# Kernel optimization log

Hardware: AMD Instinct MI355X
Metric: run time of the kernel (lower is better)

Reference implementation:

```python
import jax, jax.numpy as jnp
import numpy as np

NEG = -1e30  # log-zero surrogate (avoid -inf for stable grads)


def ctc_neg_log_like(log_probs, targets, input_lengths, target_lengths):
    """Standard CTC (blank=0) negative log-likelihood, mean over batch.
    Math-equivalent to k2 topo-compile + intersect_dense + log-semiring tot_scores.
    log_probs: [B,T,C] logits or log-probs (re-normalized, as GradExpNormalize does).
    """
    lp = jax.nn.log_softmax(log_probs, axis=-1)
    B, T, C = lp.shape
    S = targets.shape[1]
    L = 2 * S + 1  # blank-interleaved extended label sequence length
    ext = jnp.zeros((B, L), jnp.int32).at[:, 1::2].set(targets.astype(jnp.int32))
    prev2 = jnp.pad(ext[:, :-2], ((0, 0), (2, 0)), constant_values=-1)
    can_skip = (ext != prev2) & (ext != 0)  # skip transition allowed

    lp_tb = jnp.moveaxis(lp, 1, 0)  # [T,B,C] for scan over time
    start = jnp.full((B, L), NEG, lp.dtype).at[:, 0].set(0.0).at[:, 1].set(0.0)
    alpha0 = start + jnp.take_along_axis(lp_tb[0], ext, axis=1)  # [B,L]

    def step(alpha, xs):
        lp_t, t = xs
        emit_t = jnp.take_along_axis(lp_t, ext, axis=1)  # [B,L]
        s1 = jnp.pad(alpha[:, :-1], ((0, 0), (1, 0)), constant_values=NEG)
        s2 = jnp.where(can_skip,
                       jnp.pad(alpha[:, :-2], ((0, 0), (2, 0)), constant_values=NEG),
                       NEG)
        new = jnp.logaddexp(jnp.logaddexp(alpha, s1), s2) + emit_t
        # freeze alpha once past this utterance's length
        new = jnp.where((t < input_lengths)[:, None], new, alpha)
        return new, None

    ts = jnp.arange(1, T, dtype=jnp.int32)
    alpha, _ = jax.lax.scan(step, alpha0, (lp_tb[1:], ts))

    idx1 = (2 * target_lengths).astype(jnp.int32)
    idx2 = jnp.maximum(2 * target_lengths - 1, 0).astype(jnp.int32)
    a1 = jnp.take_along_axis(alpha, idx1[:, None], axis=1)[:, 0]
    a2 = jnp.take_along_axis(alpha, idx2[:, None], axis=1)[:, 0]
    a2 = jnp.where(target_lengths > 0, a2, NEG)
    tot_scores = jnp.logaddexp(a1, a2)  # per-utterance log-likelihood
    return -jnp.mean(tot_scores)  # reduction='mean'


def setup_inputs() -> dict:
    key = jax.random.key(0)
    k1, k2, k3, k4 = jax.random.split(key, 4)
    B, T, C, S = 64, 2048, 1024, 256
    log_probs = jax.random.normal(k1, (B, T, C), dtype=jnp.float32)
    targets = 1 + jax.random.randint(k2, (B, S), 0, C - 1, dtype=jnp.int32)  # labels in [1, C)
    input_lengths = jax.random.randint(k3, (B,), T // 2, T + 1, dtype=jnp.int32)
    target_lengths = jax.random.randint(k4, (B,), S // 2, S + 1, dtype=jnp.int32)
    return {"log_probs": log_probs, "targets": targets,
            "input_lengths": input_lengths, "target_lengths": target_lengths}


def reference(log_probs, targets, input_lengths, target_lengths):
    return ctc_neg_log_like(log_probs, targets, input_lengths, target_lengths)
```

## Files before the change

kernel.cpp:

```cpp
#include <hip/hip_runtime.h>
#include <math.h>

typedef __attribute__((ext_vector_type(4))) float f32x4;

#define SB() __builtin_amdgcn_sched_barrier(0)
#define WAITV(n)                                              \
  do {                                                        \
    asm volatile("s_waitcnt vmcnt(" #n ")" ::: "memory");     \
    SB();                                                     \
  } while (0)
#define LD4(dst, ptr, OFF)                                           \
  asm volatile("global_load_dwordx4 %0, %1, off offset:" OFF         \
               : "=v"(dst) : "v"(ptr) : "memory")
#define LD1(dst, ptr, OFF)                                           \
  asm volatile("global_load_dword %0, %1, off offset:" OFF           \
               : "=v"(dst) : "v"(ptr) : "memory")

__device__ inline float wave_max64(float v) {
#pragma unroll
  for (int off = 32; off > 0; off >>= 1) v = fmaxf(v, __shfl_xor(v, off, 64));
  return v;
}
__device__ inline float wave_sum64(float v) {
#pragma unroll
  for (int off = 32; off > 0; off >>= 1) v += __shfl_xor(v, off, 64);
  return v;
}
__device__ inline float wave_max_dpp(float x) {
  int xi = __float_as_int(x);
  x = fmaxf(x, __int_as_float(__builtin_amdgcn_update_dpp(xi, xi, 0x111, 0xf, 0xf, false)));
  xi = __float_as_int(x);
  x = fmaxf(x, __int_as_float(__builtin_amdgcn_update_dpp(xi, xi, 0x112, 0xf, 0xf, false)));
  xi = __float_as_int(x);
  x = fmaxf(x, __int_as_float(__builtin_amdgcn_update_dpp(xi, xi, 0x114, 0xf, 0xf, false)));
  xi = __float_as_int(x);
  x = fmaxf(x, __int_as_float(__builtin_amdgcn_update_dpp(xi, xi, 0x118, 0xf, 0xf, false)));
  xi = __float_as_int(x);
  x = fmaxf(x, __int_as_float(__builtin_amdgcn_update_dpp(xi, xi, 0x142, 0xa, 0xf, false)));
  xi = __float_as_int(x);
  x = fmaxf(x, __int_as_float(__builtin_amdgcn_update_dpp(xi, xi, 0x143, 0xc, 0xf, false)));
  return __int_as_float(__builtin_amdgcn_readlane(__float_as_int(x), 63));
}
__device__ inline float lane_shr1(float x) {
  return __int_as_float(__builtin_amdgcn_update_dpp(
      0, __float_as_int(x), 0x138, 0xf, 0xf, true));
}

__device__ __forceinline__ void k1_body(
    const float* __restrict__ lp, const int* __restrict__ targets,
    float* __restrict__ gw, int t0, int T, int Tc, int CB, int S,
    int b, int tq, float* rowbuf) {
  const int lane = threadIdx.x & 63;
  const int w = threadIdx.x >> 6;
  const int tloc = tq * 4 + w;
  const int t = t0 + tloc;
  if (t >= T) return;
  const int4 tg4 = *(const int4*)(targets + (size_t)b * S + 4 * lane);

  const float* row = lp + ((size_t)b * T + t) * 1024;
  const float4 v0 = *(const float4*)(row + 4 * lane);
  const float4 v1 = *(const float4*)(row + 256 + 4 * lane);
  const float4 v2 = *(const float4*)(row + 512 + 4 * lane);
  const float4 v3 = *(const float4*)(row + 768 + 4 * lane);
  float mx = fmaxf(fmaxf(fmaxf(v0.x, v0.y), fmaxf(v0.z, v0.w)),
                   fmaxf(fmaxf(v1.x, v1.y), fmaxf(v1.z, v1.w)));
  mx = fmaxf(mx, fmaxf(fmaxf(fmaxf(v2.x, v2.y), fmaxf(v2.z, v2.w)),
                       fmaxf(fmaxf(v3.x, v3.y), fmaxf(v3.z, v3.w))));
  mx = wave_max64(mx);
  float sm = __expf(v0.x - mx) + __expf(v0.y - mx) + __expf(v0.z - mx) +
             __expf(v0.w - mx) + __expf(v1.x - mx) + __expf(v1.y - mx) +
             __expf(v1.z - mx) + __expf(v1.w - mx) + __expf(v2.x - mx) +
             __expf(v2.y - mx) + __expf(v2.z - mx) + __expf(v2.w - mx) +
             __expf(v3.x - mx) + __expf(v3.y - mx) + __expf(v3.z - mx) +
             __expf(v3.w - mx);
  sm = wave_sum64(sm);
  const float lse = mx + __logf(sm);
  *(float4*)(rowbuf + 4 * lane) = v0;
  *(float4*)(rowbuf + 256 + 4 * lane) = v1;
  *(float4*)(rowbuf + 512 + 4 * lane) = v2;
  *(float4*)(rowbuf + 768 + 4 * lane) = v3;
  const float e0 = __expf(rowbuf[tg4.x] - lse);
  const float e1 = __expf(rowbuf[tg4.y] - lse);
  const float e2 = __expf(rowbuf[tg4.z] - lse);
  const float e3 = __expf(rowbuf[tg4.w] - lse);
  float* gr = gw + ((size_t)b * CB + tloc) * 272;
  *(float4*)(gr + 4 * lane) = make_float4(e0, e1, e2, e3);
  if (lane == 0) gr[256] = __expf(rowbuf[0] - lse);
}

__global__ __launch_bounds__(256) void k1_std(
    const float* __restrict__ lp, const int* __restrict__ targets,
    float* __restrict__ gw, int t0, int T, int Tc, int CB, int S) {
  __shared__ __align__(16) float rowbuf4[4][1024];
  k1_body(lp, targets, gw, t0, T, Tc, CB, S, blockIdx.y, blockIdx.x,
          rowbuf4[threadIdx.x >> 6]);
}

#define DECL8(P)                                                     \
  f32x4 P##v0, P##v1, P##v2, P##v3, P##v4, P##v5, P##v6, P##v7;      \
  float P##q0, P##q1, P##q2, P##q3, P##q4, P##q5, P##q6, P##q7;

#define ISS8(P)                                                      \
  do {                                                               \
    LD4(P##v0, gpA_, "0");    LD1(P##q0, gqA_, "0");                 \
    LD4(P##v1, gpA_, "1088"); LD1(P##q1, gqA_, "1088");              \
    LD4(P##v2, gpA_, "2176"); LD1(P##q2, gqA_, "2176");              \
    LD4(P##v3, gpA_, "3264"); LD1(P##q3, gqA_, "3264");              \
    LD4(P##v4, gpB_, "0");    LD1(P##q4, gqB_, "0");                 \
    LD4(P##v5, gpB_, "1088"); LD1(P##q5, gqB_, "1088");              \
    LD4(P##v6, gpB_, "2176"); LD1(P##q6, gqB_, "2176");              \
    LD4(P##v7, gpB_, "3264"); LD1(P##q7, gqB_, "3264");              \
    gpA_ += 2176; gqA_ += 2176; gpB_ += 2176; gqB_ += 2176;          \
  } while (0)

#define KSR(pv, qv)                                              \
  {                                                              \
    const float hm1 = lane_shr1(a7);                             \
    const float n0 = (a0 + hm1) * (qv);                          \
    const float n1 = __fmaf_rn(sk1, hm1, a1 + a0) * (pv).x;      \
    const float n2 = (a2 + a1) * (qv);                           \
    const float n3 = __fmaf_rn(sk3, a1, a3 + a2) * (pv).y;       \
    const float n4 = (a4 + a3) * (qv);                           \
    const float n5 = __fmaf_rn(sk5, a3, a5 + a4) * (pv).z;       \
    const float n6 = (a6 + a5) * (qv);                           \
    const float n7 = __fmaf_rn(sk7, a5, a7 + a6) * (pv).w;       \
    const float n8 = (a8 + a7) * (qv);                           \
    a0 = n0; a1 = n1; a2 = n2; a3 = n3; a4 = n4;                 \
    a5 = n5; a6 = n6; a7 = n7; a8 = n8;                          \
  }

#define RESC()                                                            \
  {                                                                       \
    float m_ = fmaxf(fmaxf(fmaxf(fmaxf(a0, a1), fmaxf(a2, a3)),           \
                           fmaxf(fmaxf(a4, a5), fmaxf(a6, a7))), a8);     \
    m_ = wave_max_dpp(m_);                                                \
    const int e_ =                                                        \
        (m_ > 0.f) ? (int)((__float_as_uint(m_) >> 23) & 255u) - 127 : 0; \
    a0 = ldexpf(a0, -e_); a1 = ldexpf(a1, -e_); a2 = ldexpf(a2, -e_);     \
    a3 = ldexpf(a3, -e_); a4 = ldexpf(a4, -e_); a5 = ldexpf(a5, -e_);     \
    a6 = ldexpf(a6, -e_); a7 = ldexpf(a7, -e_); a8 = ldexpf(a8, -e_);     \
    E += e_;                                                              \
  }

#define COMP8(P, rem)                                            \
  do {                                                           \
    if ((rem) >= 8) {                                            \
      KSR(P##v0, P##q0) KSR(P##v1, P##q1) KSR(P##v2, P##q2)      \
      KSR(P##v3, P##q3) KSR(P##v4, P##q4) KSR(P##v5, P##q5)      \
      KSR(P##v6, P##q6) KSR(P##v7, P##q7) RESC()                 \
    } else {                                                     \
      KSR(P##v0, P##q0)                                          \
      if ((rem) > 1) KSR(P##v1, P##q1)                           \
      if ((rem) > 2) KSR(P##v2, P##q2)                           \
      if ((rem) > 3) KSR(P##v3, P##q3)                           \
      if ((rem) > 4) KSR(P##v4, P##q4)                           \
      if ((rem) > 5) KSR(P##v5, P##q5)                           \
      if ((rem) > 6) KSR(P##v6, P##q6)                           \
      RESC()                                                     \
    }                                                            \
  } while (0)

template <int R0, int LAST>
__device__ __forceinline__ void k2_body(
    const float* __restrict__ gb, const int* __restrict__ targets,
    const int* __restrict__ in_len, const int* __restrict__ tgt_len,
    float* __restrict__ alpha_g, int* __restrict__ exp_g,
    float* __restrict__ tot, int b, int t0, int Tc, int S) {
  const int lane = threadIdx.x & 63;
  const int len = in_len[b];
  const int tl = tgt_len[b];
  const int* tg = targets + (size_t)b * S;
  const int4 mytg = *(const int4*)(tg + 4 * lane);
  const int tgm1 = (lane > 0) ? tg[4 * lane - 1] : -1;
  const float sk1 = (lane > 0 && mytg.x != tgm1) ? 1.f : 0.f;
  const float sk3 = (mytg.y != mytg.x) ? 1.f : 0.f;
  const float sk5 = (mytg.z != mytg.y) ? 1.f : 0.f;
  const float sk7 = (mytg.w != mytg.z) ? 1.f : 0.f;

  float a0 = 0.f, a1 = 0.f, a2 = 0.f, a3 = 0.f, a4 = 0.f, a5 = 0.f, a6 = 0.f,
        a7 = 0.f, a8 = 0.f;
  int E = 0;
  if (R0) {
    if (lane == 0) { a0 = gb[256]; a1 = gb[0]; }
  } else {
    const float* ap = alpha_g + (size_t)b * 520 + 8 * lane;
    a0 = ap[0]; a1 = ap[1]; a2 = ap[2]; a3 = ap[3];
    a4 = ap[4]; a5 = ap[5]; a6 = ap[6]; a7 = ap[7];
    a8 = (lane == 63) ? alpha_g[(size_t)b * 520 + 512] : 0.f;
    E = exp_g[b];
  }

  const int t_hi = min(t0 + Tc, len);
  int N = t_hi - (t0 + R0);
  if (N < 0) N = 0;
  const int G = (N + 7) >> 3;

  const float* gpA_ = gb + (size_t)R0 * 272 + 4 * lane;
  const float* gqA_ = gb + (size_t)R0 * 272 + 256;
  const float* gpB_ = gpA_ + 1088;
  const float* gqB_ = gqA_ + 1088;

  DECL8(A) DECL8(B)

  __builtin_amdgcn_s_setprio(1);
  asm volatile("s_waitcnt vmcnt(0) lgkmcnt(0)" ::: "memory");
  SB();
  ISS8(A); ISS8(B);

  for (int g = 0; g < G; g += 2) {
    WAITV(16);
    COMP8(A, N - 8 * g);
    ISS8(A);
    if (g + 1 < G) {
      WAITV(16);
      COMP8(B, N - 8 * (g + 1));
      ISS8(B);
    }
  }
  WAITV(0);
  __builtin_amdgcn_s_setprio(0);

  if constexpr (LAST) {
    __shared__ float fin[520];
    fin[8 * lane + 0] = a0; fin[8 * lane + 1] = a1;
    fin[8 * lane + 2] = a2; fin[8 * lane + 3] = a3;
    fin[8 * lane + 4] = a4; fin[8 * lane + 5] = a5;
    fin[8 * lane + 6] = a6; fin[8 * lane + 7] = a7;
    if (lane == 63) fin[512] = a8;
    asm volatile("s_waitcnt lgkmcnt(0)" ::: "memory");
    SB();
    if (lane == 0) {
      const int i1 = 2 * tl;
      const int i2 = (2 * tl - 1 > 0) ? (2 * tl - 1) : 0;
      float v = fin[i1] + ((tl > 0) ? fin[i2] : 0.f);
      v = fmaxf(v, 1e-37f);
      tot[b] = logf(v) + (float)E * 0.6931471805599453f;
    }
  } else {
    float* ap = alpha_g + (size_t)b * 520 + 8 * lane;
    ap[0] = a0; ap[1] = a1; ap[2] = a2; ap[3] = a3;
    ap[4] = a4; ap[5] = a5; ap[6] = a6; ap[7] = a7;
    if (lane == 63) alpha_g[(size_t)b * 520 + 512] = a8;
    if (lane == 0) exp_g[b] = E;
  }
}

template <int R0, int LAST>
__global__ __launch_bounds__(64, 1) void k2_std(
    const float* __restrict__ gbuf, const int* __restrict__ targets,
    const int* __restrict__ in_len, const int* __restrict__ tgt_len,
    float* __restrict__ alpha_g, int* __restrict__ exp_g,
    float* __restrict__ tot, int t0, int Tc, int CB, int S) {
  k2_body<R0, LAST>(gbuf + (size_t)blockIdx.x * CB * 272, targets, in_len,
                    tgt_len, alpha_g, exp_g, tot, blockIdx.x, t0, Tc, S);
}

template <int R0>
__global__ __launch_bounds__(256, 1) void fused_k(
    const float* __restrict__ lp, const int* __restrict__ targets,
    const int* __restrict__ in_len, const int* __restrict__ tgt_len,
    float* __restrict__ alpha_g, int* __restrict__ exp_g,
    float* __restrict__ tot, const float* __restrict__ gprev,
    float* __restrict__ gcur, int t0k2, int t0k1, int T, int Tc, int CB,
    int S, int TQ4) {
  __shared__ __align__(16) float rowbuf4[4][1024];
  if (blockIdx.x < 64) {
    if (threadIdx.x >= 64) return;
    k2_body<R0, 0>(gprev + (size_t)blockIdx.x * CB * 272, targets, in_len,
                   tgt_len, alpha_g, exp_g, tot, blockIdx.x, t0k2, Tc, S);
    return;
  }
  const int id = blockIdx.x - 64;
  const int b = id / TQ4;
  const int tq = id - b * TQ4;
  k1_body(lp, targets, gcur, t0k1, T, Tc, CB, S, b, tq,
          rowbuf4[threadIdx.x >> 6]);
}

__global__ void k3_mean(const float* __restrict__ tot, float* __restrict__ out,
                        int B) {
  float v = (threadIdx.x < B) ? tot[threadIdx.x] : 0.0f;
  v = wave_sum64(v);
  if (threadIdx.x == 0) out[0] = -v / (float)B;
}

extern "C" void kernel_launch(void* const* d_in, const int* in_sizes, int n_in,
                              void* d_out, int out_size, void* d_ws,
                              size_t ws_size, hipStream_t stream) {
  const float* lp = (const float*)d_in[0];
  const int* targets = (const int*)d_in[1];
  const int* in_len = (const int*)d_in[2];
  const int* tgt_len = (const int*)d_in[3];
  float* out = (float*)d_out;

  const int B = in_sizes[2];
  const int S = in_sizes[1] / B;
  const int C = 1024;
  const int T = (int)((size_t)in_sizes[0] / ((size_t)B * C));

  const size_t headf = 64 + 64 + (size_t)64 * 520;
  int Tc = 512;
  if (Tc > T) Tc = T;
  while (Tc > 64) {
    const size_t need =
        headf * 4 + 2 * (size_t)64 * (Tc + 64) * 272 * 4;
    if (need <= ws_size) break;
    Tc >>= 1;
  }
  const int CB = Tc + 64;
  const int nch = (T + Tc - 1) / Tc;
  const int TQ4 = Tc / 4;

  float* tot = (float*)d_ws;
  int* exp_g = (int*)(tot + 64);
  float* alpha_g = (float*)(exp_g + 64);
  float* g0 = alpha_g + (size_t)64 * 520;
  const size_t BUF = (size_t)64 * CB * 272;
  float* gbuf[2] = {g0, g0 + BUF};

  if (nch == 1) {
    k1_std<<<dim3(TQ4, B), 256, 0, stream>>>(lp, targets, gbuf[0], 0, T, Tc,
                                             CB, S);
    k2_std<1, 1><<<B, 64, 0, stream>>>(gbuf[0], targets, in_len, tgt_len,
                                       alpha_g, exp_g, tot, 0, Tc, CB, S);
  } else {
    k1_std<<<dim3(TQ4, B), 256, 0, stream>>>(lp, targets, gbuf[0], 0, T, Tc,
                                             CB, S);
    for (int c = 1; c < nch; ++c) {
      const int t0k2 = (c - 1) * Tc;
      const int t0k1 = c * Tc;
      const dim3 grid(64 + TQ4 * B);
      if (c == 1)
        fused_k<1><<<grid, 256, 0, stream>>>(
            lp, targets, in_len, tgt_len, alpha_g, exp_g, tot,
            gbuf[(c - 1) & 1], gbuf[c & 1], t0k2, t0k1, T, Tc, CB, S, TQ4);
      else
        fused_k<0><<<grid, 256, 0, stream>>>(
            lp, targets, in_len, tgt_len, alpha_g, exp_g, tot,
            gbuf[(c - 1) & 1], gbuf[c & 1], t0k2, t0k1, T, Tc, CB, S, TQ4);
    }
    const int cl = nch - 1;
    k2_std<0, 1><<<B, 64, 0, stream>>>(gbuf[cl & 1], targets, in_len, tgt_len,
                                       alpha_g, exp_g, tot, cl * Tc, Tc, CB,
                                       S);
  }
  k3_mean<<<1, 64, 0, stream>>>(tot, out, B);
}
```

Measured before the change: 233.5 us.

## Store gathered label probabilities as fp16 and split blank probs into separate array

The intermediate buffer of gathered emission probabilities moves from fp32 to fp16 (544-byte rows instead of 1088). Blank probabilities go into a separate contiguous fp32 array, so the recurrence loads eight of them with two vector loads instead of eight scalar loads. The aim is to halve intermediate write/read traffic and cut the load-instruction count in the serial alpha recurrence, which should shorten its latency-bound loop. The cost is fp16 precision and range on emission probabilities: very small probabilities underflow or lose precision, so the result may drift from the reference.

```diff
diff --git a/kernel.cpp b/kernel.cpp
--- a/kernel.cpp
+++ b/kernel.cpp
@@ -1,7 +1,9 @@
 #include <hip/hip_runtime.h>
+#include <hip/hip_fp16.h>
 #include <math.h>
 
 typedef __attribute__((ext_vector_type(4))) float f32x4;
+typedef __attribute__((ext_vector_type(2))) unsigned int u32x2;
 
 #define SB() __builtin_amdgcn_sched_barrier(0)
 #define WAITV(n)                                              \
@@ -9,11 +11,11 @@
     asm volatile("s_waitcnt vmcnt(" #n ")" ::: "memory");     \
     SB();                                                     \
   } while (0)
+#define LD2(dst, ptr, OFF)                                           \
+  asm volatile("global_load_dwordx2 %0, %1, off offset:" OFF         \
+               : "=v"(dst) : "v"(ptr) : "memory")
 #define LD4(dst, ptr, OFF)                                           \
   asm volatile("global_load_dwordx4 %0, %1, off offset:" OFF         \
-               : "=v"(dst) : "v"(ptr) : "memory")
-#define LD1(dst, ptr, OFF)                                           \
-  asm volatile("global_load_dword %0, %1, off offset:" OFF           \
                : "=v"(dst) : "v"(ptr) : "memory")
 
 __device__ inline float wave_max64(float v) {
@@ -48,8 +50,8 @@
 
 __device__ __forceinline__ void k1_body(
     const float* __restrict__ lp, const int* __restrict__ targets,
-    float* __restrict__ gw, int t0, int T, int Tc, int CB, int S,
-    int b, int tq, float* rowbuf) {
+    char* __restrict__ gw, float* __restrict__ qw, int t0, int T, int CB,
+    int QS, int S, int b, int tq, float* rowbuf) {
   const int lane = threadIdx.x & 63;
   const int w = threadIdx.x >> 6;
   const int tloc = tq * 4 + w;
@@ -83,50 +85,56 @@
   const float e1 = __expf(rowbuf[tg4.y] - lse);
   const float e2 = __expf(rowbuf[tg4.z] - lse);
   const float e3 = __expf(rowbuf[tg4.w] - lse);
-  float* gr = gw + ((size_t)b * CB + tloc) * 272;
-  *(float4*)(gr + 4 * lane) = make_float4(e0, e1, e2, e3);
-  if (lane == 0) gr[256] = __expf(rowbuf[0] - lse);
+  const unsigned h0 = __half_as_ushort(__float2half(e0));
+  const unsigned h1 = __half_as_ushort(__float2half(e1));
+  const unsigned h2 = __half_as_ushort(__float2half(e2));
+  const unsigned h3 = __half_as_ushort(__float2half(e3));
+  char* gr = gw + ((size_t)b * CB + tloc) * 544;
+  *(uint2*)(gr + 8 * lane) = make_uint2(h0 | (h1 << 16), h2 | (h3 << 16));
+  if (lane == 0) qw[(size_t)b * QS + tloc] = __expf(rowbuf[0] - lse);
 }
 
 __global__ __launch_bounds__(256) void k1_std(
     const float* __restrict__ lp, const int* __restrict__ targets,
-    float* __restrict__ gw, int t0, int T, int Tc, int CB, int S) {
+    char* __restrict__ gw, float* __restrict__ qw, int t0, int T, int CB,
+    int QS, int S) {
   __shared__ __align__(16) float rowbuf4[4][1024];
-  k1_body(lp, targets, gw, t0, T, Tc, CB, S, blockIdx.y, blockIdx.x,
+  k1_body(lp, targets, gw, qw, t0, T, CB, QS, S, blockIdx.y, blockIdx.x,
           rowbuf4[threadIdx.x >> 6]);
 }
 
 #define DECL8(P)                                                     \
-  f32x4 P##v0, P##v1, P##v2, P##v3, P##v4, P##v5, P##v6, P##v7;      \
-  float P##q0, P##q1, P##q2, P##q3, P##q4, P##q5, P##q6, P##q7;
+  u32x2 P##v0, P##v1, P##v2, P##v3, P##v4, P##v5, P##v6, P##v7;      \
+  f32x4 P##qL, P##qH;
 
 #define ISS8(P)                                                      \
   do {                                                               \
-    LD4(P##v0, gpA_, "0");    LD1(P##q0, gqA_, "0");                 \
-    LD4(P##v1, gpA_, "1088"); LD1(P##q1, gqA_, "1088");              \
-    LD4(P##v2, gpA_, "2176"); LD1(P##q2, gqA_, "2176");              \
-    LD4(P##v3, gpA_, "3264"); LD1(P##q3, gqA_, "3264");              \
-    LD4(P##v4, gpB_, "0");    LD1(P##q4, gqB_, "0");                 \
-    LD4(P##v5, gpB_, "1088"); LD1(P##q5, gqB_, "1088");              \
-    LD4(P##v6, gpB_, "2176"); LD1(P##q6, gqB_, "2176");              \
-    LD4(P##v7, gpB_, "3264"); LD1(P##q7, gqB_, "3264");              \
-    gpA_ += 2176; gqA_ += 2176; gpB_ += 2176; gqB_ += 2176;          \
+    LD2(P##v0, gpA_, "0");    LD2(P##v1, gpA_, "544");               \
+    LD2(P##v2, gpA_, "1088"); LD2(P##v3, gpA_, "1632");              \
+    LD2(P##v4, gpB_, "0");    LD2(P##v5, gpB_, "544");               \
+    LD2(P##v6, gpB_, "1088"); LD2(P##v7, gpB_, "1632");              \
+    LD4(P##qL, gq_, "0");     LD4(P##qH, gq_, "16");                 \
+    gpA_ += 4352; gpB_ += 4352; gq_ += 8;                            \
   } while (0)
 
-#define KSR(pv, qv)                                              \
-  {                                                              \
-    const float hm1 = lane_shr1(a7);                             \
-    const float n0 = (a0 + hm1) * (qv);                          \
-    const float n1 = __fmaf_rn(sk1, hm1, a1 + a0) * (pv).x;      \
-    const float n2 = (a2 + a1) * (qv);                           \
-    const float n3 = __fmaf_rn(sk3, a1, a3 + a2) * (pv).y;       \
-    const float n4 = (a4 + a3) * (qv);                           \
-    const float n5 = __fmaf_rn(sk5, a3, a5 + a4) * (pv).z;       \
-    const float n6 = (a6 + a5) * (qv);                           \
-    const float n7 = __fmaf_rn(sk7, a5, a7 + a6) * (pv).w;       \
-    const float n8 = (a8 + a7) * (qv);                           \
-    a0 = n0; a1 = n1; a2 = n2; a3 = n3; a4 = n4;                 \
-    a5 = n5; a6 = n6; a7 = n7; a8 = n8;                          \
+#define KSR(du, qv)                                                           \
+  {                                                                           \
+    const float px = __half2float(__ushort_as_half((unsigned short)((du).x))); \
+    const float py = __half2float(__ushort_as_half((unsigned short)((du).x >> 16))); \
+    const float pz = __half2float(__ushort_as_half((unsigned short)((du).y))); \
+    const float pw = __half2float(__ushort_as_half((unsigned short)((du).y >> 16))); \
+    const float hm1 = lane_shr1(a7);                                          \
+    const float n0 = (a0 + hm1) * (qv);                                       \
+    const float n1 = __fmaf_rn(sk1, hm1, a1 + a0) * px;                       \
+    const float n2 = (a2 + a1) * (qv);                                        \
+    const float n3 = __fmaf_rn(sk3, a1, a3 + a2) * py;                        \
+    const float n4 = (a4 + a3) * (qv);                                        \
+    const float n5 = __fmaf_rn(sk5, a3, a5 + a4) * pz;                        \
+    const float n6 = (a6 + a5) * (qv);                                        \
+    const float n7 = __fmaf_rn(sk7, a5, a7 + a6) * pw;                        \
+    const float n8 = (a8 + a7) * (qv);                                        \
+    a0 = n0; a1 = n1; a2 = n2; a3 = n3; a4 = n4;                              \
+    a5 = n5; a6 = n6; a7 = n7; a8 = n8;                                       \
   }
 
 #define RESC()                                                            \
@@ -145,27 +153,29 @@
 #define COMP8(P, rem)                                            \
   do {                                                           \
     if ((rem) >= 8) {                                            \
-      KSR(P##v0, P##q0) KSR(P##v1, P##q1) KSR(P##v2, P##q2)      \
-      KSR(P##v3, P##q3) KSR(P##v4, P##q4) KSR(P##v5, P##q5)      \
-      KSR(P##v6, P##q6) KSR(P##v7, P##q7) RESC()                 \
+      KSR(P##v0, (P##qL).x) KSR(P##v1, (P##qL).y)                \
+      KSR(P##v2, (P##qL).z) KSR(P##v3, (P##qL).w)                \
+      KSR(P##v4, (P##qH).x) KSR(P##v5, (P##qH).y)                \
+      KSR(P##v6, (P##qH).z) KSR(P##v7, (P##qH).w) RESC()         \
     } else {                                                     \
-      KSR(P##v0, P##q0)                                          \
-      if ((rem) > 1) KSR(P##v1, P##q1)                           \
-      if ((rem) > 2) KSR(P##v2, P##q2)                           \
-      if ((rem) > 3) KSR(P##v3, P##q3)                           \
-      if ((rem) > 4) KSR(P##v4, P##q4)                           \
-      if ((rem) > 5) KSR(P##v5, P##q5)                           \
-      if ((rem) > 6) KSR(P##v6, P##q6)                           \
+      KSR(P##v0, (P##qL).x)                                      \
+      if ((rem) > 1) KSR(P##v1, (P##qL).y)                       \
+      if ((rem) > 2) KSR(P##v2, (P##qL).z)                       \
+      if ((rem) > 3) KSR(P##v3, (P##qL).w)                       \
+      if ((rem) > 4) KSR(P##v4, (P##qH).x)                       \
+      if ((rem) > 5) KSR(P##v5, (P##qH).y)                       \
+      if ((rem) > 6) KSR(P##v6, (P##qH).z)                       \
       RESC()                                                     \
     }                                                            \
   } while (0)
 
 template <int R0, int LAST>
 __device__ __forceinline__ void k2_body(
-    const float* __restrict__ gb, const int* __restrict__ targets,
-    const int* __restrict__ in_len, const int* __restrict__ tgt_len,
-    float* __restrict__ alpha_g, int* __restrict__ exp_g,
-    float* __restrict__ tot, int b, int t0, int Tc, int S) {
+    const char* __restrict__ gb, const float* __restrict__ qb,
+    const int* __restrict__ targets, const int* __restrict__ in_len,
+    const int* __restrict__ tgt_len, float* __restrict__ alpha_g,
+    int* __restrict__ exp_g, float* __restrict__ tot, int b, int t0, int Tc,
+    int S) {
   const int lane = threadIdx.x & 63;
   const int len = in_len[b];
   const int tl = tgt_len[b];
@@ -181,7 +191,10 @@
         a7 = 0.f, a8 = 0.f;
   int E = 0;
   if (R0) {
-    if (lane == 0) { a0 = gb[256]; a1 = gb[0]; }
+    if (lane == 0) {
+      a0 = qb[0];
+      a1 = __half2float(*(const __half*)gb);
+    }
   } else {
     const float* ap = alpha_g + (size_t)b * 520 + 8 * lane;
     a0 = ap[0]; a1 = ap[1]; a2 = ap[2]; a3 = ap[3];
@@ -195,10 +208,9 @@
   if (N < 0) N = 0;
   const int G = (N + 7) >> 3;
 
-  const float* gpA_ = gb + (size_t)R0 * 272 + 4 * lane;
-  const float* gqA_ = gb + (size_t)R0 * 272 + 256;
-  const float* gpB_ = gpA_ + 1088;
-  const float* gqB_ = gqA_ + 1088;
+  const char* gpA_ = gb + (size_t)R0 * 544 + 8 * lane;
+  const char* gpB_ = gpA_ + 2176;
+  const float* gq_ = qb + R0;
 
   DECL8(A) DECL8(B)
 
@@ -208,11 +220,11 @@
   ISS8(A); ISS8(B);
 
   for (int g = 0; g < G; g += 2) {
-    WAITV(16);
+    WAITV(10);
     COMP8(A, N - 8 * g);
     ISS8(A);
     if (g + 1 < G) {
-      WAITV(16);
+      WAITV(10);
       COMP8(B, N - 8 * (g + 1));
       ISS8(B);
     }
@@ -247,12 +259,14 @@
 
 template <int R0, int LAST>
 __global__ __launch_bounds__(64, 1) void k2_std(
-    const float* __restrict__ gbuf, const int* __restrict__ targets,
-    const int* __restrict__ in_len, const int* __restrict__ tgt_len,
-    float* __restrict__ alpha_g, int* __restrict__ exp_g,
-    float* __restrict__ tot, int t0, int Tc, int CB, int S) {
-  k2_body<R0, LAST>(gbuf + (size_t)blockIdx.x * CB * 272, targets, in_len,
-                    tgt_len, alpha_g, exp_g, tot, blockIdx.x, t0, Tc, S);
+    const char* __restrict__ gbuf, const float* __restrict__ qbuf,
+    const int* __restrict__ targets, const int* __restrict__ in_len,
+    const int* __restrict__ tgt_len, float* __restrict__ alpha_g,
+    int* __restrict__ exp_g, float* __restrict__ tot, int t0, int Tc, int CB,
+    int QS, int S) {
+  k2_body<R0, LAST>(gbuf + (size_t)blockIdx.x * CB * 544,
+                    qbuf + (size_t)blockIdx.x * QS, targets, in_len, tgt_len,
+                    alpha_g, exp_g, tot, blockIdx.x, t0, Tc, S);
 }
 
 template <int R0>
@@ -260,20 +274,22 @@
     const float* __restrict__ lp, const int* __restrict__ targets,
     const int* __restrict__ in_len, const int* __restrict__ tgt_len,
     float* __restrict__ alpha_g, int* __restrict__ exp_g,
-    float* __restrict__ tot, const float* __restrict__ gprev,
-    float* __restrict__ gcur, int t0k2, int t0k1, int T, int Tc, int CB,
-    int S, int TQ4) {
+    float* __restrict__ tot, const char* __restrict__ gprev,
+    const float* __restrict__ qprev, char* __restrict__ gcur,
+    float* __restrict__ qcur, int t0k2, int t0k1, int T, int Tc, int CB,
+    int QS, int S, int TQ4) {
   __shared__ __align__(16) float rowbuf4[4][1024];
   if (blockIdx.x < 64) {
     if (threadIdx.x >= 64) return;
-    k2_body<R0, 0>(gprev + (size_t)blockIdx.x * CB * 272, targets, in_len,
-                   tgt_len, alpha_g, exp_g, tot, blockIdx.x, t0k2, Tc, S);
+    k2_body<R0, 0>(gprev + (size_t)blockIdx.x * CB * 544,
+                   qprev + (size_t)blockIdx.x * QS, targets, in_len, tgt_len,
+                   alpha_g, exp_g, tot, blockIdx.x, t0k2, Tc, S);
     return;
   }
   const int id = blockIdx.x - 64;
   const int b = id / TQ4;
   const int tq = id - b * TQ4;
-  k1_body(lp, targets, gcur, t0k1, T, Tc, CB, S, b, tq,
+  k1_body(lp, targets, gcur, qcur, t0k1, T, CB, QS, S, b, tq,
           rowbuf4[threadIdx.x >> 6]);
 }
 
@@ -301,31 +317,37 @@
   const size_t headf = 64 + 64 + (size_t)64 * 520;
   int Tc = 512;
   if (Tc > T) Tc = T;
-  while (Tc > 64) {
+  int CB = 0, QS = 0;
+  while (Tc >= 64) {
+    CB = Tc + 64;
+    QS = Tc + 64;
     const size_t need =
-        headf * 4 + 2 * (size_t)64 * (Tc + 64) * 272 * 4;
-    if (need <= ws_size) break;
+        (headf + 2 * (size_t)64 * QS) * 4 + 2 * (size_t)64 * CB * 544;
+    if (need <= ws_size || Tc == 64) break;
     Tc >>= 1;
   }
-  const int CB = Tc + 64;
   const int nch = (T + Tc - 1) / Tc;
   const int TQ4 = Tc / 4;
 
   float* tot = (float*)d_ws;
   int* exp_g = (int*)(tot + 64);
   float* alpha_g = (float*)(exp_g + 64);
-  float* g0 = alpha_g + (size_t)64 * 520;
-  const size_t BUF = (size_t)64 * CB * 272;
-  float* gbuf[2] = {g0, g0 + BUF};
+  float* q0 = alpha_g + (size_t)64 * 520;
+  float* q1 = q0 + (size_t)64 * QS;
+  char* g0 = (char*)(q1 + (size_t)64 * QS);
+  char* g1 = g0 + (size_t)64 * CB * 544;
+  char* gbuf[2] = {g0, g1};
+  float* qbuf[2] = {q0, q1};
 
   if (nch == 1) {
-    k1_std<<<dim3(TQ4, B), 256, 0, stream>>>(lp, targets, gbuf[0], 0, T, Tc,
-                                             CB, S);
-    k2_std<1, 1><<<B, 64, 0, stream>>>(gbuf[0], targets, in_len, tgt_len,
-                                       alpha_g, exp_g, tot, 0, Tc, CB, S);
+    k1_std<<<dim3(TQ4, B), 256, 0, stream>>>(lp, targets, gbuf[0], qbuf[0], 0,
+                                             T, CB, QS, S);
+    k2_std<1, 1><<<B, 64, 0, stream>>>(gbuf[0], qbuf[0], targets, in_len,
+                                       tgt_len, alpha_g, exp_g, tot, 0, Tc,
+                                       CB, QS, S);
   } else {
-    k1_std<<<dim3(TQ4, B), 256, 0, stream>>>(lp, targets, gbuf[0], 0, T, Tc,
-                                             CB, S);
+    k1_std<<<dim3(TQ4, B), 256, 0, stream>>>(lp, targets, gbuf[0], qbuf[0], 0,
+                                             T, CB, QS, S);
     for (int c = 1; c < nch; ++c) {
       const int t0k2 = (c - 1) * Tc;
       const int t0k1 = c * Tc;
@@ -333,16 +355,18 @@
       if (c == 1)
         fused_k<1><<<grid, 256, 0, stream>>>(
             lp, targets, in_len, tgt_len, alpha_g, exp_g, tot,
-            gbuf[(c - 1) & 1], gbuf[c & 1], t0k2, t0k1, T, Tc, CB, S, TQ4);
+            gbuf[(c - 1) & 1], qbuf[(c - 1) & 1], gbuf[c & 1], qbuf[c & 1],
+            t0k2, t0k1, T, Tc, CB, QS, S, TQ4);
       else
         fused_k<0><<<grid, 256, 0, stream>>>(
             lp, targets, in_len, tgt_len, alpha_g, exp_g, tot,
-            gbuf[(c - 1) & 1], gbuf[c & 1], t0k2, t0k1, T, Tc, CB, S, TQ4);
+            gbuf[(c - 1) & 1], qbuf[(c - 1) & 1], gbuf[c & 1], qbuf[c & 1],
+            t0k2, t0k1, T, Tc, CB, QS, S, TQ4);
     }
     const int cl = nch - 1;
-    k2_std<0, 1><<<B, 64, 0, stream>>>(gbuf[cl & 1], targets, in_len, tgt_len,
-                                       alpha_g, exp_g, tot, cl * Tc, Tc, CB,
-                                       S);
+    k2_std<0, 1><<<B, 64, 0, stream>>>(gbuf[cl & 1], qbuf[cl & 1], targets,
+                                       in_len, tgt_len, alpha_g, exp_g, tot,
+                                       cl * Tc, Tc, CB, QS, S);
   }
   k3_mean<<<1, 64, 0, stream>>>(tot, out, B);
 }
```

After: 239.6 us. 2.6% more time.
